# Kernel optimization log

Measured on AMD Instinct MI355X. Metric: run time of the kernel, lower is better.

Reference implementation:

```python
import jax, jax.numpy as jnp
import numpy as np

MAX_DISP = 4
KERNEL = 2 * MAX_DISP + 1  # 9


def setup_inputs() -> dict:
    key = jax.random.key(0)
    k1, k2 = jax.random.split(key)
    feature1 = jax.random.normal(k1, (8, 128, 128, 256), dtype=jnp.float32)
    feature2 = jax.random.normal(k2, (8, 128, 128, 256), dtype=jnp.float32)
    return {"feature1": feature1, "feature2": feature2}


def reference(feature1, feature2):
    # Windowed correlation (cost volume), equivalent to
    # unfold(feature2, k=9, pad=4) -> multiply by feature1 -> sum over channels -> /c.
    # We avoid materializing the (b, c, 81, h, w) unfolded tensor: for each of the
    # 81 displacements we slice the zero-padded feature2 and reduce over channels.
    b, c, h, w = feature1.shape
    d = MAX_DISP
    f2p = jnp.pad(feature2, ((0, 0), (0, 0), (d, d), (d, d)))  # zero padding = k//2
    corrs = []
    for ki in range(KERNEL):          # row-major kernel order, matches F.unfold
        for kj in range(KERNEL):
            shifted = f2p[:, :, ki:ki + h, kj:kj + w]          # (b, c, h, w)
            corrs.append(jnp.sum(feature1 * shifted, axis=1))  # (b, h, w)
    corr = jnp.stack(corrs, axis=1)   # (b, 81, h, w)
    return corr / c
```

## Files before the change

kernel.cpp:

```cpp
#include <hip/hip_runtime.h>


#define CT 128
#define HH 128
#define WW 256
#define NK 81
#define HW ((size_t)HH * WW)

__device__ __forceinline__ float halo_left(float x) {
    return __int_as_float(__builtin_amdgcn_update_dpp(
        0, __float_as_int(x), 0x138, 0xF, 0xF, true));
}
__device__ __forceinline__ float halo_right(float x) {
    return __int_as_float(__builtin_amdgcn_update_dpp(
        0, __float_as_int(x), 0x130, 0xF, 0xF, true));
}

__global__ __launch_bounds__(576, 4)
void corr_kernel(const float* __restrict__ f1, const float* __restrict__ f2,
                 float* __restrict__ out) {
    const int l  = threadIdx.x;
    const int wy = threadIdx.y;
    const int p  = blockIdx.x;
    const int L  = ((p & 7) << 7) | (p >> 3);
    const int b  = L >> 7;
    const int i0 = L & 127;
    const int R  = i0 - 4 + wy;

    float* op = out + ((size_t)(b * NK + wy * 9) * HH + i0) * WW + 4 * l;

    if ((unsigned)R >= (unsigned)HH) {
        const float4 z = make_float4(0.f, 0.f, 0.f, 0.f);
#pragma unroll
        for (int d = 0; d < 9; ++d) *(float4*)(op + (size_t)d * HW) = z;
        return;
    }

    const float* p1 = f1 + ((size_t)b * CT * HH + i0) * WW + 4 * l;
    const float* p2 = f2 + ((size_t)b * CT * HH + R) * WW + 4 * l;

    float acc[9][4];
#pragma unroll
    for (int d = 0; d < 9; ++d)
#pragma unroll
        for (int q = 0; q < 4; ++q) acc[d][q] = 0.f;

    for (int q = 0; q < CT / 4; ++q) {
        float4 A[4], B[4];
#pragma unroll
        for (int cc = 0; cc < 4; ++cc) {
            A[cc] = *(const float4*)(p1 + (size_t)cc * HW);
            B[cc] = *(const float4*)(p2 + (size_t)cc * HW);
        }
        p1 += 4 * HW;
        p2 += 4 * HW;
        __builtin_amdgcn_sched_barrier(0);
#pragma unroll
        for (int cc = 0; cc < 4; ++cc) {
            const float4& a = A[cc];
            const float4& r = B[cc];
            float w[12];
            w[0]  = halo_left(r.x);  w[1]  = halo_left(r.y);
            w[2]  = halo_left(r.z);  w[3]  = halo_left(r.w);
            w[4]  = r.x;             w[5]  = r.y;
            w[6]  = r.z;             w[7]  = r.w;
            w[8]  = halo_right(r.x); w[9]  = halo_right(r.y);
            w[10] = halo_right(r.z); w[11] = halo_right(r.w);
            const float fv[4] = {a.x, a.y, a.z, a.w};
#pragma unroll
            for (int d = 0; d < 9; ++d)
#pragma unroll
                for (int t = 0; t < 4; ++t)
                    acc[d][t] += fv[t] * w[t + d];
        }
    }

    const float s = 1.0f / 128.0f;
#pragma unroll
    for (int d = 0; d < 9; ++d)
        *(float4*)(op + (size_t)d * HW) =
            make_float4(acc[d][0] * s, acc[d][1] * s, acc[d][2] * s, acc[d][3] * s);
}

extern "C" void kernel_launch(void* const* d_in, const int* in_sizes, int n_in,
                              void* d_out, int out_size, void* d_ws, size_t ws_size,
                              hipStream_t stream) {
    const float* f1 = (const float*)d_in[0];
    const float* f2 = (const float*)d_in[1];
    float* out = (float*)d_out;
    dim3 grid(1024);
    dim3 block(64, 9);
    hipLaunchKernelGGL(corr_kernel, grid, block, 0, stream, f1, f2, out);
}
```

Before: 412.4 us.

## Compute three displacement rows per wave with double-buffered channel loads

Each block now has 3 waves instead of 9, and each wave accumulates three displacement rows. The feature1 load is reused across those three rows, which cuts redundant f1 reads by a factor of 3. The channel loop becomes a software-pipelined double buffer that loads channel q+1 while computing channel q. The cost is a 108-float accumulator per thread, which raises register pressure and lowers occupancy, and out-of-range rows now run predicated zero loads instead of exiting early.

```diff
diff --git a/kernel.cpp b/kernel.cpp
--- a/kernel.cpp
+++ b/kernel.cpp
@@ -16,49 +16,48 @@
         0, __float_as_int(x), 0x130, 0xF, 0xF, true));
 }
 
-__global__ __launch_bounds__(576, 4)
+__global__ __launch_bounds__(192, 3)
 void corr_kernel(const float* __restrict__ f1, const float* __restrict__ f2,
                  float* __restrict__ out) {
-    const int l  = threadIdx.x;
-    const int wy = threadIdx.y;
+    const int l  = threadIdx.x & 63;
+    const int g  = threadIdx.x >> 6;
     const int p  = blockIdx.x;
     const int L  = ((p & 7) << 7) | (p >> 3);
     const int b  = L >> 7;
     const int i0 = L & 127;
-    const int R  = i0 - 4 + wy;
 
-    float* op = out + ((size_t)(b * NK + wy * 9) * HH + i0) * WW + 4 * l;
+    const float* p1 = f1 + ((size_t)b * CT * HH + i0) * WW + 4 * l;
 
-    if ((unsigned)R >= (unsigned)HH) {
-        const float4 z = make_float4(0.f, 0.f, 0.f, 0.f);
+    bool rv[3];
+    const float* p2r[3];
 #pragma unroll
-        for (int d = 0; d < 9; ++d) *(float4*)(op + (size_t)d * HW) = z;
-        return;
+    for (int j = 0; j < 3; ++j) {
+        const int R = i0 - 4 + 3 * g + j;
+        rv[j] = ((unsigned)R < (unsigned)HH);
+        p2r[j] = f2 + ((size_t)b * CT * HH + (rv[j] ? R : 0)) * WW + 4 * l;
     }
 
-    const float* p1 = f1 + ((size_t)b * CT * HH + i0) * WW + 4 * l;
-    const float* p2 = f2 + ((size_t)b * CT * HH + R) * WW + 4 * l;
+    float acc[3][9][4];
+#pragma unroll
+    for (int j = 0; j < 3; ++j)
+#pragma unroll
+        for (int d = 0; d < 9; ++d)
+#pragma unroll
+            for (int t = 0; t < 4; ++t) acc[j][d][t] = 0.f;
 
-    float acc[9][4];
+    const float4 z4 = make_float4(0.f, 0.f, 0.f, 0.f);
+    auto LOAD = [&](int q, float4& A, float4 B[3]) {
+        A = *(const float4*)(p1 + (size_t)q * HW);
 #pragma unroll
-    for (int d = 0; d < 9; ++d)
+        for (int j = 0; j < 3; ++j)
+            B[j] = rv[j] ? *(const float4*)(p2r[j] + (size_t)q * HW) : z4;
+    };
+
+    auto COMPUTE = [&](const float4& A, const float4 B[3]) {
+        const float fv[4] = {A.x, A.y, A.z, A.w};
 #pragma unroll
-        for (int q = 0; q < 4; ++q) acc[d][q] = 0.f;
-
-    for (int q = 0; q < CT / 4; ++q) {
-        float4 A[4], B[4];
-#pragma unroll
-        for (int cc = 0; cc < 4; ++cc) {
-            A[cc] = *(const float4*)(p1 + (size_t)cc * HW);
-            B[cc] = *(const float4*)(p2 + (size_t)cc * HW);
-        }
-        p1 += 4 * HW;
-        p2 += 4 * HW;
-        __builtin_amdgcn_sched_barrier(0);
-#pragma unroll
-        for (int cc = 0; cc < 4; ++cc) {
-            const float4& a = A[cc];
-            const float4& r = B[cc];
+        for (int j = 0; j < 3; ++j) {
+            const float4& r = B[j];
             float w[12];
             w[0]  = halo_left(r.x);  w[1]  = halo_left(r.y);
             w[2]  = halo_left(r.z);  w[3]  = halo_left(r.w);
@@ -66,20 +65,36 @@
             w[6]  = r.z;             w[7]  = r.w;
             w[8]  = halo_right(r.x); w[9]  = halo_right(r.y);
             w[10] = halo_right(r.z); w[11] = halo_right(r.w);
-            const float fv[4] = {a.x, a.y, a.z, a.w};
 #pragma unroll
             for (int d = 0; d < 9; ++d)
 #pragma unroll
                 for (int t = 0; t < 4; ++t)
-                    acc[d][t] += fv[t] * w[t + d];
+                    acc[j][d][t] += fv[t] * w[t + d];
         }
+    };
+
+    float4 A0, B0[3], A1, B1[3];
+    LOAD(0, A0, B0);
+    for (int q = 0; q < CT; q += 2) {
+        LOAD(q + 1, A1, B1);
+        __builtin_amdgcn_sched_barrier(0);
+        COMPUTE(A0, B0);
+        if (q + 2 < CT) LOAD(q + 2, A0, B0);
+        __builtin_amdgcn_sched_barrier(0);
+        COMPUTE(A1, B1);
     }
 
     const float s = 1.0f / 128.0f;
 #pragma unroll
-    for (int d = 0; d < 9; ++d)
-        *(float4*)(op + (size_t)d * HW) =
-            make_float4(acc[d][0] * s, acc[d][1] * s, acc[d][2] * s, acc[d][3] * s);
+    for (int j = 0; j < 3; ++j) {
+        const int k = (3 * g + j) * 9;
+#pragma unroll
+        for (int d = 0; d < 9; ++d) {
+            float* op = out + ((size_t)(b * NK + k + d) * HH + i0) * WW + 4 * l;
+            *(float4*)op = make_float4(acc[j][d][0] * s, acc[j][d][1] * s,
+                                       acc[j][d][2] * s, acc[j][d][3] * s);
+        }
+    }
 }
 
 extern "C" void kernel_launch(void* const* d_in, const int* in_sizes, int n_in,
@@ -89,6 +104,6 @@
     const float* f2 = (const float*)d_in[1];
     float* out = (float*)d_out;
     dim3 grid(1024);
-    dim3 block(64, 9);
+    dim3 block(192);
     hipLaunchKernelGGL(corr_kernel, grid, block, 0, stream, f1, f2, out);
 }
```

Measured after the change: 1.292 ms. 213% more time.
